# Kernel optimization log

Measured on AMD Instinct MI355X. Metric: run time of the kernel, lower is better.

## Reference

```python
import jax, jax.numpy as jnp
import numpy as np

B, S, IN, H, Z = 8, 128, 64, 128, 64
N0, N1, N2 = B * S * S, B * (S // 2) ** 2, B * (S // 4) ** 2


def _grid(side, nb):
    # 4-neighbor grid, both edge directions, for nb stacked graphs
    idx = np.arange(side * side).reshape(side, side)
    h = np.stack([idx[:, :-1].ravel(), idx[:, 1:].ravel()])
    v = np.stack([idx[:-1, :].ravel(), idx[1:, :].ravel()])
    e = np.concatenate([h, v, h[::-1], v[::-1]], axis=1)  # [2, 4*side*(side-1)]
    return np.concatenate([e + g * side * side for g in range(nb)], axis=1)


def _cluster(side, nb):
    # 2x2 block clustering: (i,j) -> (i//2, j//2) on each graph
    i, j = np.meshgrid(np.arange(side), np.arange(side), indexing='ij')
    c = ((i // 2) * (side // 2) + (j // 2)).ravel()
    return np.concatenate([c + g * (side // 2) ** 2 for g in range(nb)])


def setup_inputs():
    ks = jax.random.split(jax.random.key(0), 16)

    def w(k, shape):
        return jax.random.normal(k, shape, jnp.float32) / np.float32(np.sqrt(shape[0]))

    return {
        'x': jax.random.normal(ks[0], (N0, IN), jnp.float32),
        'W_i1': w(ks[1], (IN, H)), 'b_i1': jnp.zeros((H,), jnp.float32),
        'W_i2': w(ks[2], (H, H)), 'b_i2': jnp.zeros((H,), jnp.float32),
        'W_b0a': w(ks[3], (H, H)), 'b_b0a': jnp.zeros((H,), jnp.float32),
        'W_b0b': w(ks[4], (H, H)), 'b_b0b': jnp.zeros((H,), jnp.float32),
        'W_b1a': w(ks[5], (H, H)), 'b_b1a': jnp.zeros((H,), jnp.float32),
        'W_b1b': w(ks[6], (H, H)), 'b_b1b': jnp.zeros((H,), jnp.float32),
        'W_mu': w(ks[7], (H, Z)), 'b_mu': jnp.zeros((Z,), jnp.float32),
        'W_lv': w(ks[8], (H, Z)), 'b_lv': jnp.zeros((Z,), jnp.float32),
        'edge_index0': jnp.asarray(_grid(S, B), jnp.int32),
        'edge_index1': jnp.asarray(_grid(S // 2, B), jnp.int32),
        'cluster0': jnp.asarray(_cluster(S, B), jnp.int32),
        'cluster1': jnp.asarray(_cluster(S // 2, B), jnp.int32),
        'batch2': jnp.asarray(np.repeat(np.arange(B), (S // 4) ** 2), jnp.int32),
    }


def _gcn(x, W, b, src, dst, n):
    # PyG GCNConv: add self-loops, symmetric D^-1/2 (A+I) D^-1/2 normalization
    h = x @ W
    loop = jnp.arange(n, dtype=src.dtype)
    s = jnp.concatenate([src, loop])
    d = jnp.concatenate([dst, loop])
    deg = jax.ops.segment_sum(jnp.ones(s.shape, x.dtype), d, num_segments=n)
    dinv = jax.lax.rsqrt(deg)  # deg >= 1 thanks to self-loops
    msg = h[s] * (dinv[s] * dinv[d])[:, None]  # [E+n, H]
    return jax.ops.segment_sum(msg, d, num_segments=n) + b


def reference(x, W_i1, b_i1, W_i2, b_i2, W_b0a, b_b0a, W_b0b, b_b0b,
              W_b1a, b_b1a, W_b1b, b_b1b, W_mu, b_mu, W_lv, b_lv,
              edge_index0, edge_index1, cluster0, cluster1, batch2):
    r = jax.nn.relu
    s0, d0 = edge_index0[0], edge_index0[1]
    h = r(_gcn(x, W_i1, b_i1, s0, d0, N0))
    h = r(_gcn(h, W_i2, b_i2, s0, d0, N0))
    # RG block 0: two GCN layers then graclus/max_pool coarsening (2x2 blocks)
    h = r(_gcn(h, W_b0a, b_b0a, s0, d0, N0))
    h = r(_gcn(h, W_b0b, b_b0b, s0, d0, N0))
    h = jax.ops.segment_max(h, cluster0, num_segments=N1)
    # RG block 1 on the coarse grid
    s1, d1 = edge_index1[0], edge_index1[1]
    h = r(_gcn(h, W_b1a, b_b1a, s1, d1, N1))
    h = r(_gcn(h, W_b1b, b_b1b, s1, d1, N1))
    h = jax.ops.segment_max(h, cluster1, num_segments=N2)
    # global mean pool per graph at the final level
    sums = jax.ops.segment_sum(h, batch2, num_segments=B)
    cnt = jax.ops.segment_sum(jnp.ones((h.shape[0], 1), h.dtype), batch2, num_segments=B)
    hg = sums / cnt  # [B, H]
    return hg @ W_mu + b_mu, hg @ W_lv + b_lv
```

## Files before the change

### kernel.cpp

```cpp
#include <hip/hip_runtime.h>
#include <hip/hip_bf16.h>
#include <stdint.h>

#define BG 8
#define HD 128
#define NN0 131072
#define NN1 32768
#define NN2 8192

typedef __attribute__((ext_vector_type(8))) _Float16 f16x8;
typedef __attribute__((ext_vector_type(4))) float f32x4;
typedef __attribute__((ext_vector_type(8))) unsigned short u16x8;

__device__ __forceinline__ float dinv_sel(int deg) {
    return deg == 3 ? 0.5773502691896258f : (deg == 4 ? 0.5f : 0.4472135954999579f);
}
template <int S>
__device__ __forceinline__ float dinv_ij(int i, int j) {
    const int deg = 1 + (i > 0) + (i < S - 1) + (j > 0) + (j < S - 1);
    return dinv_sel(deg);
}

__global__ __launch_bounds__(256) void pack_weights_kernel(
    const float* __restrict__ W0, const float* __restrict__ W1,
    const float* __restrict__ W2, const float* __restrict__ W3,
    const float* __restrict__ W4, const float* __restrict__ W5,
    _Float16* __restrict__ Wp)
{
    const int e = blockIdx.x * 256 + threadIdx.x;
    if (e >= 90112) return;
    const float* src; int K, off, p;
    if (e < 8192) { src = W0; K = 64; off = 0; p = e; }
    else {
        const int q = e - 8192; const int w = q >> 14; p = q & 16383;
        K = 128; off = 16384 + w * 32768;
        src = (w == 0) ? W1 : (w == 1) ? W2 : (w == 2) ? W3 : (w == 3) ? W4 : W5;
    }
    const int el = p & 7;
    const int lane = (p >> 3) & 63;
    const int ctkc = p >> 9;
    const int ct = ctkc & 7;
    const int kc = ctkc >> 3;
    const int k = kc * 32 + (lane >> 4) * 8 + el;
    const int col = ct * 16 + (lane & 15);
    const float f = src[k * 128 + col];
    const _Float16 hi = (_Float16)f;
    Wp[off + p] = hi;
    Wp[off + K * 128 + p] = (_Float16)((f - (float)hi) * 64.0f);
}

__global__ __launch_bounds__(256) void repack_kernel(
    const float* __restrict__ x, _Float16* __restrict__ P)
{
    const int id = blockIdx.x * 256 + threadIdx.x;
    const int node = id >> 3;
    const int q = id & 7;
    const int j = node & 127, i = (node >> 7) & 127;
    const float dv = dinv_ij<128>(i, j);
    const float4 v0 = *reinterpret_cast<const float4*>(&x[(size_t)node * 64 + q * 8]);
    const float4 v1 = *reinterpret_cast<const float4*>(&x[(size_t)node * 64 + q * 8 + 4]);
    union { _Float16 h[8]; uint4 u; } o;
    o.h[0] = (_Float16)(v0.x * dv); o.h[1] = (_Float16)(v0.y * dv);
    o.h[2] = (_Float16)(v0.z * dv); o.h[3] = (_Float16)(v0.w * dv);
    o.h[4] = (_Float16)(v1.x * dv); o.h[5] = (_Float16)(v1.y * dv);
    o.h[6] = (_Float16)(v1.z * dv); o.h[7] = (_Float16)(v1.w * dv);
    *reinterpret_cast<uint4*>(&P[((size_t)q * NN0 + node) * 8]) = o.u;
}

template <int K, int SLOG, bool PRESCALE_OUT>
__global__ __launch_bounds__(256, 4) void fused_gcn4_kernel(
    const _Float16* __restrict__ Xp, const _Float16* __restrict__ Wa,
    const float* __restrict__ bias, _Float16* __restrict__ Hh)
{
    constexpr int S = 1 << SLOG;
    constexpr int N = BG * S * S;
    constexpr int NCH = K / 32;
    constexpr int LDSH = (K * 128 > 4 * 16 * 136) ? K * 128 : 4 * 16 * 136;
    __shared__ alignas(16) _Float16 Ls[LDSH];

    const int tid  = threadIdx.x;
    const int lane = tid & 63;
    const int wv   = tid >> 6;
    const int lr   = lane & 15;
    const int lq   = lane >> 4;

    for (int s = tid; s < K * 16; s += 256)
        *reinterpret_cast<uint4*>(&Ls[(size_t)s * 8]) =
            *reinterpret_cast<const uint4*>(&Wa[(size_t)s * 8]);

    const int bswz = ((blockIdx.x & 7) * ((int)gridDim.x >> 3)) + (blockIdx.x >> 3);
    const int n0   = bswz * 64 + wv * 16;
    const int node = n0 + lr;
    const int j = node & (S - 1);
    const int i = (node >> SLOG) & (S - 1);
    const float dvd = dinv_ij<S>(i, j);
    const float fl = (j > 0) ? 1.f : 0.f;
    const float fr = (j < S - 1) ? 1.f : 0.f;
    const float fu = (i > 0) ? 1.f : 0.f;
    const float fd = (i < S - 1) ? 1.f : 0.f;
    const int oL = (j > 0) ? -8 : 0;
    const int oR = (j < S - 1) ? 8 : 0;
    const int oU = (i > 0) ? -8 * S : 0;
    const int oD = (i < S - 1) ? 8 * S : 0;

    f32x4 acc[8];
#pragma unroll
    for (int c = 0; c < 8; ++c) acc[c] = (f32x4){0.f, 0.f, 0.f, 0.f};

    __syncthreads();

#pragma unroll
    for (int ch = 0; ch < NCH; ++ch) {
        const _Float16* bp = &Xp[((size_t)((ch << 2) + lq) * N + node) * 8];
        const f16x8 c8 = *reinterpret_cast<const f16x8*>(bp);
        const f16x8 l8 = *reinterpret_cast<const f16x8*>(bp + oL);
        const f16x8 r8 = *reinterpret_cast<const f16x8*>(bp + oR);
        const f16x8 u8 = *reinterpret_cast<const f16x8*>(bp + oU);
        const f16x8 d8 = *reinterpret_cast<const f16x8*>(bp + oD);
        f16x8 bf;
#pragma unroll
        for (int e2 = 0; e2 < 8; ++e2) {
            float y = (float)c8[e2];
            y = fmaf(fl, (float)l8[e2], y);
            y = fmaf(fr, (float)r8[e2], y);
            y = fmaf(fu, (float)u8[e2], y);
            y = fmaf(fd, (float)d8[e2], y);
            bf[e2] = (_Float16)(y * dvd);
        }
#pragma unroll
        for (int ct = 0; ct < 8; ++ct) {
            const f16x8 wf = *reinterpret_cast<const f16x8*>(
                &Ls[(size_t)(((ch << 3) + ct) * 64 + lane) * 8]);
            acc[ct] = __builtin_amdgcn_mfma_f32_16x16x32_f16(wf, bf, acc[ct], 0, 0, 0);
        }
    }

    const float dvo = PRESCALE_OUT ? dvd : 1.f;
    __syncthreads();
    _Float16* Et = &Ls[wv * (16 * 136)];
#pragma unroll
    for (int ct = 0; ct < 8; ++ct) {
        const float4 bv = *reinterpret_cast<const float4*>(&bias[ct * 16 + lq * 4]);
        const float bb[4] = {bv.x, bv.y, bv.z, bv.w};
#pragma unroll
        for (int t = 0; t < 4; ++t) {
            const float v = fmaxf(acc[ct][t] + bb[t], 0.f) * dvo;
            Et[lr * 136 + ct * 16 + lq * 4 + t] = (_Float16)v;
        }
    }
    __syncthreads();
#pragma unroll
    for (int p = 0; p < 4; ++p) {
        const int kc2 = lq + (p << 2);
        const f16x8 vv = *reinterpret_cast<const f16x8*>(&Et[lr * 136 + kc2 * 8]);
        *reinterpret_cast<f16x8*>(&Hh[((size_t)kc2 * N + n0 + lr) * 8]) = vv;
    }
}

template <int SLOG_OUT, bool SCALE>
__global__ __launch_bounds__(256) void pool_kernel(
    const _Float16* __restrict__ Hin, _Float16* __restrict__ O)
{
    constexpr int sc = 1 << SLOG_OUT;
    constexpr int Nout = BG * sc * sc;
    constexpr int Nin = Nout * 4;
    constexpr int sideIn = sc * 2;
    const int id = blockIdx.x * 256 + threadIdx.x;
    const int kc = id / Nout;
    const int n  = id & (Nout - 1);
    const int cj = n & (sc - 1);
    const int ci = (n >> SLOG_OUT) & (sc - 1);
    const int g  = n >> (2 * SLOG_OUT);
    const int nin = (g * sideIn + 2 * ci) * sideIn + 2 * cj;
    const _Float16* base = &Hin[((size_t)kc * Nin + nin) * 8];
    const u16x8 a = *reinterpret_cast<const u16x8*>(base);
    const u16x8 b = *reinterpret_cast<const u16x8*>(base + 8);
    const u16x8 c = *reinterpret_cast<const u16x8*>(base + (size_t)sideIn * 8);
    const u16x8 d = *reinterpret_cast<const u16x8*>(base + (size_t)sideIn * 8 + 8);
    u16x8 o;
#pragma unroll
    for (int e = 0; e < 8; ++e) {
        const unsigned short m1 = a[e] > b[e] ? a[e] : b[e];
        const unsigned short m2 = c[e] > d[e] ? c[e] : d[e];
        o[e] = m1 > m2 ? m1 : m2;
    }
    if (SCALE) {
        const float dv = dinv_ij<sc>(ci, cj);
#pragma unroll
        for (int e = 0; e < 8; ++e) {
            union { unsigned short u; _Float16 h; } t; t.u = o[e];
            t.h = (_Float16)((float)t.h * dv);
            o[e] = t.u;
        }
    }
    *reinterpret_cast<u16x8*>(&O[((size_t)kc * Nout + n) * 8]) = o;
}

__global__ __launch_bounds__(256) void meanpool_kernel(
    const _Float16* __restrict__ Hin, float* __restrict__ hg)
{
    __shared__ float Lp[256][8];
    const int g  = blockIdx.x >> 4;
    const int kc = blockIdx.x & 15;
    const int t  = threadIdx.x;
    float s[8] = {0.f, 0.f, 0.f, 0.f, 0.f, 0.f, 0.f, 0.f};
    for (int n = t; n < 1024; n += 256) {
        const f16x8 v = *reinterpret_cast<const f16x8*>(
            &Hin[((size_t)kc * NN2 + g * 1024 + n) * 8]);
#pragma unroll
        for (int e = 0; e < 8; ++e) s[e] += (float)v[e];
    }
#pragma unroll
    for (int e = 0; e < 8; ++e) Lp[t][e] = s[e];
    __syncthreads();
    for (int st = 128; st >= 1; st >>= 1) {
        if (t < st) {
#pragma unroll
            for (int e = 0; e < 8; ++e) Lp[t][e] += Lp[t + st][e];
        }
        __syncthreads();
    }
    if (t < 8) hg[g * HD + kc * 8 + t] = Lp[0][t] * (1.f / 1024.f);
}

__global__ __launch_bounds__(512) void head_kernel(
    const float* __restrict__ hg,
    const float* __restrict__ Wmu, const float* __restrict__ bmu,
    const float* __restrict__ Wlv, const float* __restrict__ blv,
    float* __restrict__ out)
{
    const int t = threadIdx.x;
    const int r = t >> 6;
    const int c = t & 63;
    float s1 = 0.f, s2 = 0.f;
#pragma unroll 8
    for (int k = 0; k < HD; ++k) {
        const float x = hg[r * HD + k];
        s1 = fmaf(x, Wmu[k * 64 + c], s1);
        s2 = fmaf(x, Wlv[k * 64 + c], s2);
    }
    out[r * 64 + c] = s1 + bmu[c];
    out[512 + r * 64 + c] = s2 + blv[c];
}

extern "C" void kernel_launch(void* const* d_in, const int* in_sizes, int n_in,
                              void* d_out, int out_size, void* d_ws, size_t ws_size,
                              hipStream_t stream) {
    const float* x     = (const float*)d_in[0];
    const float* W_i1  = (const float*)d_in[1];
    const float* b_i1  = (const float*)d_in[2];
    const float* W_i2  = (const float*)d_in[3];
    const float* b_i2  = (const float*)d_in[4];
    const float* W_b0a = (const float*)d_in[5];
    const float* b_b0a = (const float*)d_in[6];
    const float* W_b0b = (const float*)d_in[7];
    const float* b_b0b = (const float*)d_in[8];
    const float* W_b1a = (const float*)d_in[9];
    const float* b_b1a = (const float*)d_in[10];
    const float* W_b1b = (const float*)d_in[11];
    const float* b_b1b = (const float*)d_in[12];
    const float* W_mu  = (const float*)d_in[13];
    const float* b_mu  = (const float*)d_in[14];
    const float* W_lv  = (const float*)d_in[15];
    const float* b_lv  = (const float*)d_in[16];

    _Float16* Wp   = (_Float16*)d_ws;
    _Float16* P    = (_Float16*)((char*)d_ws + 524288);
    _Float16* bufA = (_Float16*)((char*)d_ws + 524288 + 16777216);
    _Float16* bufB = bufA + (size_t)NN0 * HD;
    float*    hg   = (float*)(bufB + (size_t)NN0 * HD);

    const _Float16* Wp_i1  = Wp;
    const _Float16* Wp_i2  = Wp + 16384;
    const _Float16* Wp_b0a = Wp + 16384 + 1 * 32768;
    const _Float16* Wp_b0b = Wp + 16384 + 2 * 32768;
    const _Float16* Wp_b1a = Wp + 16384 + 3 * 32768;
    const _Float16* Wp_b1b = Wp + 16384 + 4 * 32768;

    pack_weights_kernel<<<352, 256, 0, stream>>>(
        W_i1, W_i2, W_b0a, W_b0b, W_b1a, W_b1b, Wp);
    repack_kernel<<<NN0 * 8 / 256, 256, 0, stream>>>(x, P);

    fused_gcn4_kernel<64, 7, true ><<<NN0 / 64, 256, 0, stream>>>(P,    Wp_i1,  b_i1,  bufA);
    fused_gcn4_kernel<128, 7, true ><<<NN0 / 64, 256, 0, stream>>>(bufA, Wp_i2,  b_i2,  bufB);
    fused_gcn4_kernel<128, 7, true ><<<NN0 / 64, 256, 0, stream>>>(bufB, Wp_b0a, b_b0a, bufA);
    fused_gcn4_kernel<128, 7, false><<<NN0 / 64, 256, 0, stream>>>(bufA, Wp_b0b, b_b0b, bufB);

    pool_kernel<6, true><<<NN1 * 16 / 256, 256, 0, stream>>>(bufB, bufA);

    fused_gcn4_kernel<128, 6, true ><<<NN1 / 64, 256, 0, stream>>>(bufA, Wp_b1a, b_b1a, bufB);
    fused_gcn4_kernel<128, 6, false><<<NN1 / 64, 256, 0, stream>>>(bufB, Wp_b1b, b_b1b, bufA);

    pool_kernel<5, false><<<NN2 * 16 / 256, 256, 0, stream>>>(bufA, bufB);

    meanpool_kernel<<<BG * 16, 256, 0, stream>>>(bufB, hg);

    head_kernel<<<1, 512, 0, stream>>>(hg, W_mu, b_mu, W_lv, b_lv, (float*)d_out);
}
```

Baseline: 119.2 us.

## Fuse input repack and max-pools into GCN kernels, drop LDS staging

Measured after the change: 139.6 us. +17.1%, slower.

```diff
diff --git a/kernel.cpp b/kernel.cpp
--- a/kernel.cpp
+++ b/kernel.cpp
@@ -10,7 +10,6 @@
 
 typedef __attribute__((ext_vector_type(8))) _Float16 f16x8;
 typedef __attribute__((ext_vector_type(4))) float f32x4;
-typedef __attribute__((ext_vector_type(8))) unsigned short u16x8;
 
 __device__ __forceinline__ float dinv_sel(int deg) {
     return deg == 3 ? 0.5773502691896258f : (deg == 4 ? 0.5f : 0.4472135954999579f);
@@ -29,11 +28,11 @@
 {
     const int e = blockIdx.x * 256 + threadIdx.x;
     if (e >= 90112) return;
-    const float* src; int K, off, p;
-    if (e < 8192) { src = W0; K = 64; off = 0; p = e; }
+    const float* src; int off, p;
+    if (e < 8192) { src = W0; off = 0; p = e; }
     else {
         const int q = e - 8192; const int w = q >> 14; p = q & 16383;
-        K = 128; off = 16384 + w * 32768;
+        off = 16384 + w * 32768;
         src = (w == 0) ? W1 : (w == 1) ? W2 : (w == 2) ? W3 : (w == 3) ? W4 : W5;
     }
     const int el = p & 7;
@@ -43,50 +42,23 @@
     const int kc = ctkc >> 3;
     const int k = kc * 32 + (lane >> 4) * 8 + el;
     const int col = ct * 16 + (lane & 15);
-    const float f = src[k * 128 + col];
-    const _Float16 hi = (_Float16)f;
-    Wp[off + p] = hi;
-    Wp[off + K * 128 + p] = (_Float16)((f - (float)hi) * 64.0f);
-}
-
-__global__ __launch_bounds__(256) void repack_kernel(
-    const float* __restrict__ x, _Float16* __restrict__ P)
-{
-    const int id = blockIdx.x * 256 + threadIdx.x;
-    const int node = id >> 3;
-    const int q = id & 7;
-    const int j = node & 127, i = (node >> 7) & 127;
-    const float dv = dinv_ij<128>(i, j);
-    const float4 v0 = *reinterpret_cast<const float4*>(&x[(size_t)node * 64 + q * 8]);
-    const float4 v1 = *reinterpret_cast<const float4*>(&x[(size_t)node * 64 + q * 8 + 4]);
-    union { _Float16 h[8]; uint4 u; } o;
-    o.h[0] = (_Float16)(v0.x * dv); o.h[1] = (_Float16)(v0.y * dv);
-    o.h[2] = (_Float16)(v0.z * dv); o.h[3] = (_Float16)(v0.w * dv);
-    o.h[4] = (_Float16)(v1.x * dv); o.h[5] = (_Float16)(v1.y * dv);
-    o.h[6] = (_Float16)(v1.z * dv); o.h[7] = (_Float16)(v1.w * dv);
-    *reinterpret_cast<uint4*>(&P[((size_t)q * NN0 + node) * 8]) = o.u;
-}
-
-template <int K, int SLOG, bool PRESCALE_OUT>
-__global__ __launch_bounds__(256, 4) void fused_gcn4_kernel(
-    const _Float16* __restrict__ Xp, const _Float16* __restrict__ Wa,
+    Wp[off + p] = (_Float16)src[k * 128 + col];
+}
+
+template <int K, int SLOG, bool PRESCALE_OUT, int MODE>
+__global__ __launch_bounds__(256, 4) void fused_gcn5_kernel(
+    const void* __restrict__ Xv, const _Float16* __restrict__ Wa,
     const float* __restrict__ bias, _Float16* __restrict__ Hh)
 {
     constexpr int S = 1 << SLOG;
     constexpr int N = BG * S * S;
     constexpr int NCH = K / 32;
-    constexpr int LDSH = (K * 128 > 4 * 16 * 136) ? K * 128 : 4 * 16 * 136;
-    __shared__ alignas(16) _Float16 Ls[LDSH];
 
     const int tid  = threadIdx.x;
     const int lane = tid & 63;
     const int wv   = tid >> 6;
     const int lr   = lane & 15;
     const int lq   = lane >> 4;
-
-    for (int s = tid; s < K * 16; s += 256)
-        *reinterpret_cast<uint4*>(&Ls[(size_t)s * 8]) =
-            *reinterpret_cast<const uint4*>(&Wa[(size_t)s * 8]);
 
     const int bswz = ((blockIdx.x & 7) * ((int)gridDim.x >> 3)) + (blockIdx.x >> 3);
     const int n0   = bswz * 64 + wv * 16;
@@ -94,109 +66,125 @@
     const int j = node & (S - 1);
     const int i = (node >> SLOG) & (S - 1);
     const float dvd = dinv_ij<S>(i, j);
+
+    const int oL = (j > 0) ? -8 : 0;
+    const int oR = (j < S - 1) ? 8 : 0;
+    const int oU = (i > 0) ? -8 * S : 0;
+    const int oD = (i < S - 1) ? 8 * S : 0;
     const float fl = (j > 0) ? 1.f : 0.f;
     const float fr = (j < S - 1) ? 1.f : 0.f;
     const float fu = (i > 0) ? 1.f : 0.f;
     const float fd = (i < S - 1) ? 1.f : 0.f;
-    const int oL = (j > 0) ? -8 : 0;
-    const int oR = (j < S - 1) ? 8 : 0;
-    const int oU = (i > 0) ? -8 * S : 0;
-    const int oD = (i < S - 1) ? 8 * S : 0;
+    float w5[5];
+    w5[0] = dvd;
+    w5[1] = (j > 0)     ? dinv_ij<S>(i, j - 1) : 0.f;
+    w5[2] = (j < S - 1) ? dinv_ij<S>(i, j + 1) : 0.f;
+    w5[3] = (i > 0)     ? dinv_ij<S>(i - 1, j) : 0.f;
+    w5[4] = (i < S - 1) ? dinv_ij<S>(i + 1, j) : 0.f;
+    int t1o[5];
+    t1o[0] = 0;
+    t1o[1] = (j > 0) ? -K : 0;
+    t1o[2] = (j < S - 1) ? K : 0;
+    t1o[3] = (i > 0) ? -K * S : 0;
+    t1o[4] = (i < S - 1) ? K * S : 0;
+    int t2b[5];
+    {
+        const int g2 = node >> (2 * SLOG);
+        auto fbase = [&](int ti, int tj) {
+            return (g2 * 4 * S * S + ti * 4 * S + tj * 2) * 8;
+        };
+        t2b[0] = fbase(i, j);
+        t2b[1] = (j > 0) ? fbase(i, j - 1) : t2b[0];
+        t2b[2] = (j < S - 1) ? fbase(i, j + 1) : t2b[0];
+        t2b[3] = (i > 0) ? fbase(i - 1, j) : t2b[0];
+        t2b[4] = (i < S - 1) ? fbase(i + 1, j) : t2b[0];
+    }
 
     f32x4 acc[8];
 #pragma unroll
     for (int c = 0; c < 8; ++c) acc[c] = (f32x4){0.f, 0.f, 0.f, 0.f};
 
-    __syncthreads();
-
 #pragma unroll
     for (int ch = 0; ch < NCH; ++ch) {
-        const _Float16* bp = &Xp[((size_t)((ch << 2) + lq) * N + node) * 8];
-        const f16x8 c8 = *reinterpret_cast<const f16x8*>(bp);
-        const f16x8 l8 = *reinterpret_cast<const f16x8*>(bp + oL);
-        const f16x8 r8 = *reinterpret_cast<const f16x8*>(bp + oR);
-        const f16x8 u8 = *reinterpret_cast<const f16x8*>(bp + oU);
-        const f16x8 d8 = *reinterpret_cast<const f16x8*>(bp + oD);
+        const int q = (ch << 2) + lq;
         f16x8 bf;
-#pragma unroll
-        for (int e2 = 0; e2 < 8; ++e2) {
-            float y = (float)c8[e2];
-            y = fmaf(fl, (float)l8[e2], y);
-            y = fmaf(fr, (float)r8[e2], y);
-            y = fmaf(fu, (float)u8[e2], y);
-            y = fmaf(fd, (float)d8[e2], y);
-            bf[e2] = (_Float16)(y * dvd);
+        if constexpr (MODE == 0) {
+            const _Float16* bp = &((const _Float16*)Xv)[((size_t)q * N + node) * 8];
+            const f16x8 c8 = *reinterpret_cast<const f16x8*>(bp);
+            const f16x8 l8 = *reinterpret_cast<const f16x8*>(bp + oL);
+            const f16x8 r8 = *reinterpret_cast<const f16x8*>(bp + oR);
+            const f16x8 u8 = *reinterpret_cast<const f16x8*>(bp + oU);
+            const f16x8 d8 = *reinterpret_cast<const f16x8*>(bp + oD);
+#pragma unroll
+            for (int e = 0; e < 8; ++e) {
+                float y = (float)c8[e];
+                y = fmaf(fl, (float)l8[e], y);
+                y = fmaf(fr, (float)r8[e], y);
+                y = fmaf(fu, (float)u8[e], y);
+                y = fmaf(fd, (float)d8[e], y);
+                bf[e] = (_Float16)(y * dvd);
+            }
+        } else if constexpr (MODE == 1) {
+            const float* xb = &((const float*)Xv)[(size_t)node * K + q * 8];
+            float y[8] = {0.f, 0.f, 0.f, 0.f, 0.f, 0.f, 0.f, 0.f};
+#pragma unroll
+            for (int t = 0; t < 5; ++t) {
+                const float4 a = *reinterpret_cast<const float4*>(xb + t1o[t]);
+                const float4 b = *reinterpret_cast<const float4*>(xb + t1o[t] + 4);
+                const float w = w5[t];
+                y[0] = fmaf(a.x, w, y[0]); y[1] = fmaf(a.y, w, y[1]);
+                y[2] = fmaf(a.z, w, y[2]); y[3] = fmaf(a.w, w, y[3]);
+                y[4] = fmaf(b.x, w, y[4]); y[5] = fmaf(b.y, w, y[5]);
+                y[6] = fmaf(b.z, w, y[6]); y[7] = fmaf(b.w, w, y[7]);
+            }
+#pragma unroll
+            for (int e = 0; e < 8; ++e) bf[e] = (_Float16)(y[e] * dvd);
+        } else {
+            const _Float16* pl = &((const _Float16*)Xv)[(size_t)q * (4 * N) * 8];
+            float y[8] = {0.f, 0.f, 0.f, 0.f, 0.f, 0.f, 0.f, 0.f};
+#pragma unroll
+            for (int t = 0; t < 5; ++t) {
+                const _Float16* fb = pl + t2b[t];
+                const f16x8 p00 = *reinterpret_cast<const f16x8*>(fb);
+                const f16x8 p01 = *reinterpret_cast<const f16x8*>(fb + 8);
+                const f16x8 p10 = *reinterpret_cast<const f16x8*>(fb + 16 * S);
+                const f16x8 p11 = *reinterpret_cast<const f16x8*>(fb + 16 * S + 8);
+                const float w = w5[t];
+#pragma unroll
+                for (int e = 0; e < 8; ++e) {
+                    const _Float16 m1 = p00[e] > p01[e] ? p00[e] : p01[e];
+                    const _Float16 m2 = p10[e] > p11[e] ? p10[e] : p11[e];
+                    const _Float16 m = m1 > m2 ? m1 : m2;
+                    y[e] = fmaf((float)m, w, y[e]);
+                }
+            }
+#pragma unroll
+            for (int e = 0; e < 8; ++e) bf[e] = (_Float16)(y[e] * dvd);
         }
 #pragma unroll
         for (int ct = 0; ct < 8; ++ct) {
             const f16x8 wf = *reinterpret_cast<const f16x8*>(
-                &Ls[(size_t)(((ch << 3) + ct) * 64 + lane) * 8]);
+                &Wa[(size_t)(((ch << 3) + ct) * 64 + lane) * 8]);
             acc[ct] = __builtin_amdgcn_mfma_f32_16x16x32_f16(wf, bf, acc[ct], 0, 0, 0);
         }
     }
 
     const float dvo = PRESCALE_OUT ? dvd : 1.f;
-    __syncthreads();
-    _Float16* Et = &Ls[wv * (16 * 136)];
 #pragma unroll
     for (int ct = 0; ct < 8; ++ct) {
         const float4 bv = *reinterpret_cast<const float4*>(&bias[ct * 16 + lq * 4]);
         const float bb[4] = {bv.x, bv.y, bv.z, bv.w};
-#pragma unroll
-        for (int t = 0; t < 4; ++t) {
-            const float v = fmaxf(acc[ct][t] + bb[t], 0.f) * dvo;
-            Et[lr * 136 + ct * 16 + lq * 4 + t] = (_Float16)v;
-        }
-    }
-    __syncthreads();
-#pragma unroll
-    for (int p = 0; p < 4; ++p) {
-        const int kc2 = lq + (p << 2);
-        const f16x8 vv = *reinterpret_cast<const f16x8*>(&Et[lr * 136 + kc2 * 8]);
-        *reinterpret_cast<f16x8*>(&Hh[((size_t)kc2 * N + n0 + lr) * 8]) = vv;
-    }
-}
-
-template <int SLOG_OUT, bool SCALE>
-__global__ __launch_bounds__(256) void pool_kernel(
-    const _Float16* __restrict__ Hin, _Float16* __restrict__ O)
-{
-    constexpr int sc = 1 << SLOG_OUT;
-    constexpr int Nout = BG * sc * sc;
-    constexpr int Nin = Nout * 4;
-    constexpr int sideIn = sc * 2;
-    const int id = blockIdx.x * 256 + threadIdx.x;
-    const int kc = id / Nout;
-    const int n  = id & (Nout - 1);
-    const int cj = n & (sc - 1);
-    const int ci = (n >> SLOG_OUT) & (sc - 1);
-    const int g  = n >> (2 * SLOG_OUT);
-    const int nin = (g * sideIn + 2 * ci) * sideIn + 2 * cj;
-    const _Float16* base = &Hin[((size_t)kc * Nin + nin) * 8];
-    const u16x8 a = *reinterpret_cast<const u16x8*>(base);
-    const u16x8 b = *reinterpret_cast<const u16x8*>(base + 8);
-    const u16x8 c = *reinterpret_cast<const u16x8*>(base + (size_t)sideIn * 8);
-    const u16x8 d = *reinterpret_cast<const u16x8*>(base + (size_t)sideIn * 8 + 8);
-    u16x8 o;
-#pragma unroll
-    for (int e = 0; e < 8; ++e) {
-        const unsigned short m1 = a[e] > b[e] ? a[e] : b[e];
-        const unsigned short m2 = c[e] > d[e] ? c[e] : d[e];
-        o[e] = m1 > m2 ? m1 : m2;
-    }
-    if (SCALE) {
-        const float dv = dinv_ij<sc>(ci, cj);
-#pragma unroll
-        for (int e = 0; e < 8; ++e) {
-            union { unsigned short u; _Float16 h; } t; t.u = o[e];
-            t.h = (_Float16)((float)t.h * dv);
-            o[e] = t.u;
-        }
-    }
-    *reinterpret_cast<u16x8*>(&O[((size_t)kc * Nout + n) * 8]) = o;
-}
-
-__global__ __launch_bounds__(256) void meanpool_kernel(
+        union { _Float16 h[4]; uint2 u; } o;
+#pragma unroll
+        for (int t = 0; t < 4; ++t)
+            o.h[t] = (_Float16)(fmaxf(acc[ct][t] + bb[t], 0.f) * dvo);
+        const int kc2 = (ct << 1) + (lq >> 1);
+        *reinterpret_cast<uint2*>(
+            &Hh[((size_t)kc2 * N + node) * 8 + (lq & 1) * 4]) = o.u;
+    }
+}
+
+__global__ __launch_bounds__(256) void poolmean_kernel(
     const _Float16* __restrict__ Hin, float* __restrict__ hg)
 {
     __shared__ float Lp[256][8];
@@ -204,11 +192,23 @@
     const int kc = blockIdx.x & 15;
     const int t  = threadIdx.x;
     float s[8] = {0.f, 0.f, 0.f, 0.f, 0.f, 0.f, 0.f, 0.f};
-    for (int n = t; n < 1024; n += 256) {
-        const f16x8 v = *reinterpret_cast<const f16x8*>(
-            &Hin[((size_t)kc * NN2 + g * 1024 + n) * 8]);
-#pragma unroll
-        for (int e = 0; e < 8; ++e) s[e] += (float)v[e];
+    const _Float16* pl = &Hin[(size_t)kc * NN1 * 8];
+#pragma unroll
+    for (int p = 0; p < 4; ++p) {
+        const int n2 = t + (p << 8);
+        const int ci = n2 >> 5, cj = n2 & 31;
+        const int nf = g * 4096 + ci * 128 + cj * 2;
+        const _Float16* fb = pl + (size_t)nf * 8;
+        const f16x8 p00 = *reinterpret_cast<const f16x8*>(fb);
+        const f16x8 p01 = *reinterpret_cast<const f16x8*>(fb + 8);
+        const f16x8 p10 = *reinterpret_cast<const f16x8*>(fb + 512);
+        const f16x8 p11 = *reinterpret_cast<const f16x8*>(fb + 520);
+#pragma unroll
+        for (int e = 0; e < 8; ++e) {
+            const _Float16 m1 = p00[e] > p01[e] ? p00[e] : p01[e];
+            const _Float16 m2 = p10[e] > p11[e] ? p10[e] : p11[e];
+            s[e] += (float)(m1 > m2 ? m1 : m2);
+        }
     }
 #pragma unroll
     for (int e = 0; e < 8; ++e) Lp[t][e] = s[e];
@@ -265,8 +265,7 @@
     const float* b_lv  = (const float*)d_in[16];
 
     _Float16* Wp   = (_Float16*)d_ws;
-    _Float16* P    = (_Float16*)((char*)d_ws + 524288);
-    _Float16* bufA = (_Float16*)((char*)d_ws + 524288 + 16777216);
+    _Float16* bufA = (_Float16*)((char*)d_ws + 524288);
     _Float16* bufB = bufA + (size_t)NN0 * HD;
     float*    hg   = (float*)(bufB + (size_t)NN0 * HD);
 
@@ -279,21 +278,16 @@
 
     pack_weights_kernel<<<352, 256, 0, stream>>>(
         W_i1, W_i2, W_b0a, W_b0b, W_b1a, W_b1b, Wp);
-    repack_kernel<<<NN0 * 8 / 256, 256, 0, stream>>>(x, P);
-
-    fused_gcn4_kernel<64, 7, true ><<<NN0 / 64, 256, 0, stream>>>(P,    Wp_i1,  b_i1,  bufA);
-    fused_gcn4_kernel<128, 7, true ><<<NN0 / 64, 256, 0, stream>>>(bufA, Wp_i2,  b_i2,  bufB);
-    fused_gcn4_kernel<128, 7, true ><<<NN0 / 64, 256, 0, stream>>>(bufB, Wp_b0a, b_b0a, bufA);
-    fused_gcn4_kernel<128, 7, false><<<NN0 / 64, 256, 0, stream>>>(bufA, Wp_b0b, b_b0b, bufB);
-
-    pool_kernel<6, true><<<NN1 * 16 / 256, 256, 0, stream>>>(bufB, bufA);
-
-    fused_gcn4_kernel<128, 6, true ><<<NN1 / 64, 256, 0, stream>>>(bufA, Wp_b1a, b_b1a, bufB);
-    fused_gcn4_kernel<128, 6, false><<<NN1 / 64, 256, 0, stream>>>(bufB, Wp_b1b, b_b1b, bufA);
-
-    pool_kernel<5, false><<<NN2 * 16 / 256, 256, 0, stream>>>(bufA, bufB);
-
-    meanpool_kernel<<<BG * 16, 256, 0, stream>>>(bufB, hg);
+
+    fused_gcn5_kernel<64, 7, true, 1 ><<<NN0 / 64, 256, 0, stream>>>(x,    Wp_i1,  b_i1,  bufA);
+    fused_gcn5_kernel<128, 7, true, 0 ><<<NN0 / 64, 256, 0, stream>>>(bufA, Wp_i2,  b_i2,  bufB);
+    fused_gcn5_kernel<128, 7, true, 0 ><<<NN0 / 64, 256, 0, stream>>>(bufB, Wp_b0a, b_b0a, bufA);
+    fused_gcn5_kernel<128, 7, false, 0><<<NN0 / 64, 256, 0, stream>>>(bufA, Wp_b0b, b_b0b, bufB);
+
+    fused_gcn5_kernel<128, 6, true, 2 ><<<NN1 / 64, 256, 0, stream>>>(bufB, Wp_b1a, b_b1a, bufA);
+    fused_gcn5_kernel<128, 6, false, 0><<<NN1 / 64, 256, 0, stream>>>(bufA, Wp_b1b, b_b1b, bufB);
+
+    poolmean_kernel<<<BG * 16, 256, 0, stream>>>(bufB, hg);
 
     head_kernel<<<1, 512, 0, stream>>>(hg, W_mu, b_mu, W_lv, b_lv, (float*)d_out);
 }
```
